# Optimization experiments

Measured on AMD Instinct MI355X. Metric: run time of the kernel, lower is better.

The kernel has to match this reference:

```python
import jax, jax.numpy as jnp
import numpy as np
from jax import lax

B, C_IN, H, W = 16, 2048, 16, 16
HIDDEN, N_ANC = 512, 9
N_POS, N_NEG = 2048, 2048
TOT = B * N_ANC * H * W  # 36864 = flat conf logits; also rows of reg.view(-1,4)


def _xyxy_to_cxcywh(b):
    x1, y1, x2, y2 = b[..., 0], b[..., 1], b[..., 2], b[..., 3]
    return jnp.stack([(x1 + x2) * 0.5, (y1 + y2) * 0.5, x2 - x1, y2 - y1], axis=-1)


def _cxcywh_to_xyxy(b):
    cx, cy, w, h = b[..., 0], b[..., 1], b[..., 2], b[..., 3]
    return jnp.stack([cx - w * 0.5, cy - h * 0.5, cx + w * 0.5, cy + h * 0.5], axis=-1)


def _rand_boxes(key, n):
    # valid xyxy boxes on the 16x16 feature-map coordinate grid, w,h in [1,4]
    k1, k2 = jax.random.split(key)
    xy = jax.random.uniform(k1, (n, 2), jnp.float32) * 12.0
    wh = 1.0 + jax.random.uniform(k2, (n, 2), jnp.float32) * 3.0
    return jnp.concatenate([xy, xy + wh], axis=-1)


def setup_inputs() -> dict:
    key = jax.random.key(0)
    ks = jax.random.split(key, 10)
    feature_map = jax.random.normal(ks[0], (B, C_IN, H, W), jnp.float32)
    pos_anc_ind = jax.random.randint(ks[1], (N_POS,), 0, TOT)
    neg_anc_ind = jax.random.randint(ks[2], (N_NEG,), 0, TOT)
    pos_anc_coords = _rand_boxes(ks[3], N_POS)
    gt_bboxes_pos = _rand_boxes(ks[4], N_POS)
    s1 = 1.0 / np.sqrt(C_IN * 9)
    W1 = jax.random.uniform(ks[5], (HIDDEN, C_IN, 3, 3), jnp.float32, -s1, s1)
    b1 = jnp.zeros((HIDDEN,), jnp.float32)
    s2 = 1.0 / np.sqrt(HIDDEN)
    Wc = jax.random.uniform(ks[6], (N_ANC, HIDDEN), jnp.float32, -s2, s2)
    bc = jnp.zeros((N_ANC,), jnp.float32)
    Wr = jax.random.uniform(ks[7], (N_ANC * 4, HIDDEN), jnp.float32, -s2, s2)
    br = jnp.zeros((N_ANC * 4,), jnp.float32)
    return {"feature_map": feature_map, "pos_anc_coords": pos_anc_coords,
            "gt_bboxes_pos": gt_bboxes_pos, "W1": W1, "b1": b1, "Wc": Wc,
            "bc": bc, "Wr": Wr, "br": br,
            "pos_anc_ind": pos_anc_ind, "neg_anc_ind": neg_anc_ind}


def generate_proposals(anchors, offsets):
    a = _xyxy_to_cxcywh(anchors)
    p = jnp.stack([a[:, 0] + offsets[:, 0] * a[:, 2],
                   a[:, 1] + offsets[:, 1] * a[:, 3],
                   a[:, 2] * jnp.exp(offsets[:, 2]),
                   a[:, 3] * jnp.exp(offsets[:, 3])], axis=-1)
    return _cxcywh_to_xyxy(p)


def calc_gt_offsets(anc, gt):
    a = _xyxy_to_cxcywh(anc)
    g = _xyxy_to_cxcywh(gt)
    tx = (g[:, 0] - a[:, 0]) / a[:, 2]
    ty = (g[:, 1] - a[:, 1]) / a[:, 3]
    tw = jnp.log(g[:, 2] / a[:, 2])
    th = jnp.log(g[:, 3] / a[:, 3])
    return jnp.stack([tx, ty, tw, th], axis=-1)


def reference(feature_map, pos_anc_coords, gt_bboxes_pos, W1, b1, Wc, bc, Wr, br,
              pos_anc_ind, neg_anc_ind):
    # ProposalModule: conv3x3 -> (dropout=identity in eval) -> relu -> 1x1 heads
    out = lax.conv_general_dilated(feature_map, W1, (1, 1), 'SAME',
                                   dimension_numbers=('NCHW', 'OIHW', 'NCHW'))
    out = jax.nn.relu(out + b1[None, :, None, None])
    conf = jnp.einsum('bchw,oc->bohw', out, Wc) + bc[None, :, None, None]   # [B,9,H,W]
    reg = jnp.einsum('bchw,oc->bohw', out, Wr) + br[None, :, None, None]    # [B,36,H,W]
    # irregular flat gathers, exactly mirroring torch .flatten()/.view(-1,4)
    conf_pos = conf.reshape(-1)[pos_anc_ind]
    conf_neg = conf.reshape(-1)[neg_anc_ind]
    offsets_pos = reg.reshape(-1, 4)[pos_anc_ind]
    proposals = generate_proposals(pos_anc_coords, offsets_pos)
    gt_offsets = calc_gt_offsets(pos_anc_coords, gt_bboxes_pos)
    # BCE-with-logits, targets 1 for pos / 0 for neg, reduction='sum' / B
    cls_loss = (jnp.sum(jax.nn.softplus(-conf_pos)) + jnp.sum(jax.nn.softplus(conf_neg))) / B
    # smooth L1 (beta=1), reduction='sum' / B
    d = offsets_pos - gt_offsets
    ad = jnp.abs(d)
    reg_loss = jnp.sum(jnp.where(ad < 1.0, 0.5 * d * d, ad - 0.5)) / B
    total_rpn_loss = 1.0 * cls_loss + 5.0 * reg_loss  # w_conf=1, w_reg=5
    return total_rpn_loss, proposals
```

## Files before the change

kernel.cpp:

```cpp
#include <hip/hip_runtime.h>
#include <hip/hip_bf16.h>
#include <stdint.h>

#define CIN 2048
#define HID 512
#define NPOS 2048
#define NNEG 2048

#define BM 256
#define BN 256
#define BK 32
#define NS 8
#define A_ELEMS (BM * BK)
#define B_ELEMS (BN * BK)

typedef __attribute__((ext_vector_type(8))) short s16x8;
typedef __attribute__((ext_vector_type(4))) short s16x4;
typedef __attribute__((ext_vector_type(4))) float f32x4;
typedef unsigned short ushort_t;

static __device__ __forceinline__ float bf2f(unsigned short u) {
    union { float f; unsigned int i; } v; v.i = ((unsigned int)u) << 16; return v.f;
}
static __device__ __forceinline__ unsigned short f2bf(float f) {
    union { float f; unsigned int i; } v; v.f = f;
    unsigned int r = v.i + 0x7FFF + ((v.i >> 16) & 1);
    return (unsigned short)(r >> 16);
}

typedef __attribute__((address_space(1))) const void gvoid_t;
typedef __attribute__((address_space(3))) void lvoid_t;
static __device__ __forceinline__ void gload16(const void* g, void* l) {
    __builtin_amdgcn_global_load_lds((gvoid_t*)g, (lvoid_t*)l, 16, 0, 0);
}

__global__ __launch_bounds__(256) void k_prep(const float* __restrict__ F,
                                              const float* __restrict__ W1,
                                              ushort_t* __restrict__ Fp,
                                              ushort_t* __restrict__ Wt2) {
    __shared__ float tile[64][17];
    __shared__ float buf[512 * 9];
    int bid = blockIdx.x;
    int t = threadIdx.x;
    if (bid < 256) {
        int b = bid >> 4, y = bid & 15;
        for (int ic0 = 0; ic0 < CIN; ic0 += 64) {
            {
                int ci = t >> 2, xg = t & 3;
                const float4 v = *(const float4*)&F[((size_t)(b * CIN + ic0 + ci) * 16 + y) * 16 + xg * 4];
                tile[ci][xg * 4 + 0] = v.x;
                tile[ci][xg * 4 + 1] = v.y;
                tile[ci][xg * 4 + 2] = v.z;
                tile[ci][xg * 4 + 3] = v.w;
            }
            __syncthreads();
            {
                int x = t >> 4, cig = t & 15;
                s16x4 o;
#pragma unroll
                for (int j = 0; j < 4; ++j) o[j] = (short)f2bf(tile[cig * 4 + j][x]);
                *(s16x4*)&Fp[((size_t)(b * 18 + y + 1) * 18 + (x + 1)) * CIN + ic0 + cig * 4] = o;
            }
            __syncthreads();
        }
    } else if (bid < 768) {
        int oc = bid - 256;
        for (int ic0 = 0; ic0 < CIN; ic0 += 512) {
            const float* src = W1 + ((size_t)oc * CIN + ic0) * 9;
            for (int i = t; i < 512 * 9; i += 256) buf[i] = src[i];
            __syncthreads();
            for (int s = t; s < 9 * 64; s += 256) {
                int k = s >> 6, g = s & 63;
                s16x8 v;
#pragma unroll
                for (int j = 0; j < 8; ++j) v[j] = (short)f2bf(buf[(g * 8 + j) * 9 + k]);
                *(s16x8*)&Wt2[((size_t)(k * HID + oc)) * CIN + ic0 + g * 8] = v;
            }
            __syncthreads();
        }
    } else {
        const s16x8 z = {0, 0, 0, 0, 0, 0, 0, 0};
        for (int idx = (bid - 768) * 256 + t; idx < 16 * 68 * 256; idx += 64 * 256) {
            int seg = idx & 255;
            int cell = (idx >> 8) % 68;
            int b = idx / (68 * 256);
            int Y, X;
            if (cell < 18)      { Y = 0;         X = cell; }
            else if (cell < 36) { Y = 17;        X = cell - 18; }
            else if (cell < 52) { Y = cell - 35; X = 0; }
            else                { Y = cell - 51; X = 17; }
            *(s16x8*)&Fp[((size_t)(b * 18 + Y) * 18 + X) * CIN + seg * 8] = z;
        }
    }
}

__global__ __launch_bounds__(512, 2) void k_gemm(const ushort_t* __restrict__ Fp,
                                                 const ushort_t* __restrict__ Wt2,
                                                 ushort_t* __restrict__ Part,
                                                 int icLen, int nPairs) {
    extern __shared__ ushort_t ldsbuf[];
    ushort_t* As = ldsbuf;
    ushort_t* Bs = ldsbuf + 4 * A_ELEMS;

    int bid = blockIdx.x;
    int rb = bid / nPairs;
    int pair = bid - rb * nPairs;
    int split = pair >> 1, cb = pair & 1;
    int icBase = split * icLen;
    int m0 = rb * BM, oc0 = cb * BN;
    int t = threadIdx.x;
    int wid = t >> 6, lane = t & 63;
    int wr = wid >> 2, wn = wid & 3;
    int hi = lane >> 4, lo = lane & 15;

    f32x4 acc[8][4];
#pragma unroll
    for (int a = 0; a < 8; ++a)
#pragma unroll
        for (int b = 0; b < 4; ++b) acc[a][b] = (f32x4){0.f, 0.f, 0.f, 0.f};

    int Abase[2], Bbase[2];
#pragma unroll
    for (int j = 0; j < 2; ++j) {
        int li = j * 512 + t;
        int row = li >> 2;
        int sg = (li & 3) ^ ((row >> 1) & 3);
        int m = m0 + row;
        int b = m >> 8, y = (m >> 4) & 15, x = m & 15;
        Abase[j] = ((b * 18 + y) * 18 + x) * CIN + sg * 8;
        Bbase[j] = (oc0 + row) * CIN + sg * 8;
    }
    int aidx[8], bidx[4];
#pragma unroll
    for (int fm = 0; fm < 8; ++fm) {
        int r = wr * 128 + fm * 16 + lo;
        aidx[fm] = r * BK + ((hi ^ ((r >> 1) & 3)) << 3);
    }
#pragma unroll
    for (int fn = 0; fn < 4; ++fn) {
        int rB = wn * 64 + fn * 16 + lo;
        bidx[fn] = rB * BK + ((hi ^ ((rB >> 1) & 3)) << 3);
    }

    const int nsteps = (icLen / BK) * 9;

#define STAGE(BUF, S)                                                                \
    do {                                                                             \
        int kidx_ = (S) % 9, icc_ = (S) / 9;                                         \
        int ak_ = ((kidx_ / 3) * 18 + (kidx_ - 3 * (kidx_ / 3))) * CIN + icBase + icc_ * BK; \
        int bk_ = kidx_ * HID * CIN + icBase + icc_ * BK;                            \
        ushort_t* dA_ = As + (BUF) * A_ELEMS;                                        \
        ushort_t* dB_ = Bs + (BUF) * B_ELEMS;                                        \
        _Pragma("unroll") for (int j_ = 0; j_ < 2; ++j_) {                           \
            gload16(Fp + Abase[j_] + ak_, dA_ + (size_t)(j_ * 512 + t) * 8);         \
            gload16(Wt2 + Bbase[j_] + bk_, dB_ + (size_t)(j_ * 512 + t) * 8);        \
        }                                                                            \
    } while (0)

    STAGE(0, 0); STAGE(1, 1); STAGE(2, 2);
    asm volatile("s_waitcnt vmcnt(8)" ::: "memory");
    __builtin_amdgcn_s_barrier();
    __builtin_amdgcn_sched_barrier(0);

#pragma unroll 1
    for (int step = 0; step < nsteps; ++step) {
        const ushort_t* cA = As + (step & 3) * A_ELEMS;
        const ushort_t* cB = Bs + (step & 3) * B_ELEMS;
        if (step + 3 < nsteps) STAGE((step + 3) & 3, step + 3);
        s16x8 af[8], bf[4];
#pragma unroll
        for (int fm = 0; fm < 8; ++fm) af[fm] = *(const s16x8*)&cA[aidx[fm]];
#pragma unroll
        for (int fn = 0; fn < 4; ++fn) bf[fn] = *(const s16x8*)&cB[bidx[fn]];
        __builtin_amdgcn_s_setprio(1);
#pragma unroll
        for (int fm = 0; fm < 8; ++fm)
#pragma unroll
            for (int fn = 0; fn < 4; ++fn)
                acc[fm][fn] = __builtin_amdgcn_mfma_f32_16x16x32_bf16(
                    af[fm], bf[fn], acc[fm][fn], 0, 0, 0);
        __builtin_amdgcn_s_setprio(0);
        if (step + 3 < nsteps) {
            asm volatile("s_waitcnt vmcnt(8)" ::: "memory");
            __builtin_amdgcn_s_barrier();
            __builtin_amdgcn_sched_barrier(0);
        } else if (step + 1 < nsteps) {
            asm volatile("s_waitcnt vmcnt(0)" ::: "memory");
            __builtin_amdgcn_s_barrier();
            __builtin_amdgcn_sched_barrier(0);
        }
    }
#undef STAGE

#pragma unroll
    for (int fm = 0; fm < 8; ++fm)
#pragma unroll
        for (int fn = 0; fn < 4; ++fn)
#pragma unroll
            for (int r = 0; r < 4; ++r) {
                int gm = m0 + wr * 128 + fm * 16 + hi * 4 + r;
                int gn = oc0 + wn * 64 + fn * 16 + lo;
                Part[((size_t)split * 4096 + gm) * HID + gn] = f2bf(acc[fm][fn][r]);
            }
}

__global__ __launch_bounds__(256) void k_heads(const ushort_t* __restrict__ Part, int ns,
                                               const float* __restrict__ b1,
                                               const float* __restrict__ Wc,
                                               const float* __restrict__ bc,
                                               const float* __restrict__ Wr,
                                               const float* __restrict__ br,
                                               float* __restrict__ conf,
                                               float* __restrict__ reg) {
    extern __shared__ ushort_t hsm[];
    ushort_t* Ah = hsm;
    ushort_t* Wh = hsm + 16 * HID;
    int t = threadIdx.x;
    int wid = t >> 6, lane = t & 63;
    int hi = lane >> 4, lo = lane & 15;
    int row0 = blockIdx.x * 16;

#pragma unroll
    for (int i = 0; i < 4; ++i) {
        int pos = i * 256 + t;
        int r = pos >> 6, sg = pos & 63;
        float s[8];
#pragma unroll
        for (int j = 0; j < 8; ++j) s[j] = 0.f;
        for (int sp = 0; sp < ns; ++sp) {
            s16x8 v = *(const s16x8*)&Part[((size_t)sp * 4096 + row0 + r) * HID + sg * 8];
#pragma unroll
            for (int j = 0; j < 8; ++j) s[j] += bf2f((unsigned short)v[j]);
        }
        s16x8 o;
#pragma unroll
        for (int j = 0; j < 8; ++j) o[j] = (short)f2bf(fmaxf(s[j] + b1[sg * 8 + j], 0.f));
        *(s16x8*)&Ah[r * HID + ((sg ^ (r & 7)) << 3)] = o;
    }
#pragma unroll
    for (int i = 0; i < 12; ++i) {
        int sid = i * 256 + t;
        int o = sid >> 6, sg = sid & 63;
        s16x8 v;
#pragma unroll
        for (int j = 0; j < 8; ++j) {
            float w = 0.f;
            if (o < 9) w = Wc[o * HID + sg * 8 + j];
            else if (o < 45) w = Wr[(size_t)(o - 9) * HID + sg * 8 + j];
            v[j] = (short)f2bf(w);
        }
        *(s16x8*)&Wh[o * HID + ((sg ^ (o & 7)) << 3)] = v;
    }
    __syncthreads();
    if (wid != 0) return;

    f32x4 acc[3];
#pragma unroll
    for (int fn = 0; fn < 3; ++fn) acc[fn] = (f32x4){0.f, 0.f, 0.f, 0.f};
#pragma unroll 1
    for (int kf = 0; kf < 16; ++kf) {
        int rA = lo;
        s16x8 a_ = *(const s16x8*)&Ah[rA * HID + ((kf * 32 + hi * 8) ^ ((rA & 7) << 3))];
#pragma unroll
        for (int fn = 0; fn < 3; ++fn) {
            int rB = fn * 16 + lo;
            s16x8 b_ = *(const s16x8*)&Wh[rB * HID + ((kf * 32 + hi * 8) ^ ((rB & 7) << 3))];
            acc[fn] = __builtin_amdgcn_mfma_f32_16x16x32_bf16(a_, b_, acc[fn], 0, 0, 0);
        }
    }
#pragma unroll
    for (int fn = 0; fn < 3; ++fn)
#pragma unroll
        for (int r = 0; r < 4; ++r) {
            int gm = row0 + hi * 4 + r;
            int o = fn * 16 + lo;
            float v = acc[fn][r];
            if (o < 9) conf[gm * 9 + o] = v + bc[o];
            else if (o < 45) reg[gm * 36 + (o - 9)] = v + br[o - 9];
        }
}

static __device__ __forceinline__ float softplus(float x) {
    return log1pf(expf(-fabsf(x))) + fmaxf(x, 0.f);
}

__global__ __launch_bounds__(1024) void k_loss(const float* __restrict__ conf,
                                               const float* __restrict__ reg,
                                               const int* __restrict__ pos_ind,
                                               const int* __restrict__ neg_ind,
                                               const float* __restrict__ anc,
                                               const float* __restrict__ gt,
                                               float* __restrict__ out) {
    int t = threadIdx.x;
    float cls = 0.f, rloss = 0.f;
    for (int p = t; p < NPOS; p += 1024) {
        int ind = pos_ind[p];
        {
            int b = ind / 2304, r = ind % 2304;
            int c = r >> 8, r2 = r & 255;
            float cv = conf[(b * 256 + r2) * 9 + c];
            cls += softplus(-cv);
        }
        float off[4];
#pragma unroll
        for (int j = 0; j < 4; ++j) {
            int e = 4 * ind + j;
            int b = e / 9216, r = e % 9216;
            int c = r >> 8, r2 = r & 255;
            off[j] = reg[(b * 256 + r2) * 36 + c];
        }
        float ax1 = anc[4 * p], ay1 = anc[4 * p + 1], ax2 = anc[4 * p + 2], ay2 = anc[4 * p + 3];
        float acx = (ax1 + ax2) * 0.5f, acy = (ay1 + ay2) * 0.5f;
        float aw = ax2 - ax1, ah = ay2 - ay1;
        float pcx = acx + off[0] * aw, pcy = acy + off[1] * ah;
        float pw = aw * expf(off[2]), ph = ah * expf(off[3]);
        out[1 + 4 * p + 0] = pcx - pw * 0.5f;
        out[1 + 4 * p + 1] = pcy - ph * 0.5f;
        out[1 + 4 * p + 2] = pcx + pw * 0.5f;
        out[1 + 4 * p + 3] = pcy + ph * 0.5f;
        float gx1 = gt[4 * p], gy1 = gt[4 * p + 1], gx2 = gt[4 * p + 2], gy2 = gt[4 * p + 3];
        float gcx = (gx1 + gx2) * 0.5f, gcy = (gy1 + gy2) * 0.5f;
        float gw = gx2 - gx1, gh = gy2 - gy1;
        float tv[4];
        tv[0] = (gcx - acx) / aw;
        tv[1] = (gcy - acy) / ah;
        tv[2] = logf(gw / aw);
        tv[3] = logf(gh / ah);
#pragma unroll
        for (int j = 0; j < 4; ++j) {
            float d = off[j] - tv[j];
            float ad = fabsf(d);
            rloss += (ad < 1.f) ? 0.5f * d * d : ad - 0.5f;
        }
    }
    for (int q = t; q < NNEG; q += 1024) {
        int ind = neg_ind[q];
        int b = ind / 2304, r = ind % 2304;
        int c = r >> 8, r2 = r & 255;
        float cv = conf[(b * 256 + r2) * 9 + c];
        cls += softplus(cv);
    }
    __shared__ float s1[1024], s2[1024];
    s1[t] = cls;
    s2[t] = rloss;
    __syncthreads();
    for (int s = 512; s > 0; s >>= 1) {
        if (t < s) {
            s1[t] += s1[t + s];
            s2[t] += s2[t + s];
        }
        __syncthreads();
    }
    if (t == 0) out[0] = (s1[0] + 5.f * s2[0]) / 16.f;
}

extern "C" void kernel_launch(void* const* d_in, const int* in_sizes, int n_in,
                              void* d_out, int out_size, void* d_ws, size_t ws_size,
                              hipStream_t stream) {
    const float* F   = (const float*)d_in[0];
    const float* anc = (const float*)d_in[1];
    const float* gt  = (const float*)d_in[2];
    const float* W1  = (const float*)d_in[3];
    const float* b1  = (const float*)d_in[4];
    const float* Wc  = (const float*)d_in[5];
    const float* bc  = (const float*)d_in[6];
    const float* Wr  = (const float*)d_in[7];
    const float* br  = (const float*)d_in[8];
    const int* pos_ind = (const int*)d_in[9];
    const int* neg_ind = (const int*)d_in[10];
    float* out = (float*)d_out;

    char* ws = (char*)d_ws;
    const size_t FP_BYTES   = (size_t)16 * 18 * 18 * CIN * 2;
    const size_t WT_BYTES   = (size_t)9 * HID * CIN * 2;
    const size_t PART_ONE   = (size_t)4096 * HID * 2;
    const size_t CONF_BYTES = (size_t)4096 * 9 * 4;

    int icLen = CIN / NS;

    ushort_t* Fp   = (ushort_t*)ws;
    ushort_t* Wt2  = (ushort_t*)(ws + FP_BYTES);
    ushort_t* Part = (ushort_t*)(ws + FP_BYTES + WT_BYTES);
    float* conf    = (float*)(ws + FP_BYTES + WT_BYTES + (size_t)NS * PART_ONE);
    float* reg     = (float*)(ws + FP_BYTES + WT_BYTES + (size_t)NS * PART_ONE + CONF_BYTES);

    const int GEMM_LDS = 4 * (A_ELEMS + B_ELEMS) * 2;
    hipFuncSetAttribute((const void*)k_gemm, hipFuncAttributeMaxDynamicSharedMemorySize, GEMM_LDS);
    const int HEADS_LDS = (16 + 48) * HID * 2;
    hipFuncSetAttribute((const void*)k_heads, hipFuncAttributeMaxDynamicSharedMemorySize, HEADS_LDS);

    k_prep<<<832, 256, 0, stream>>>(F, W1, Fp, Wt2);
    k_gemm<<<(4096 / BM) * (HID / BN) * NS, 512, GEMM_LDS, stream>>>(Fp, Wt2, Part, icLen, 2 * NS);
    k_heads<<<256, 256, HEADS_LDS, stream>>>(Part, NS, b1, Wc, bc, Wr, br, conf, reg);
    k_loss<<<1, 1024, 0, stream>>>(conf, reg, pos_ind, neg_ind, anc, gt, out);
}
```

Measured before the change: 134.5 us.

## Restructure conv GEMM main loop: BK=64 double buffer with interleaved quarter-stage loads

Doubles the K tile to 64 and drops from a 4-deep to a 2-deep LDS ring, keeping the same LDS footprint. Each step is split into four MFMA phases, and each phase is fenced by barriers and paired with one quarter of the next tile's global-to-LDS loads. The LDS swizzle changes to an 8-way XOR pattern to suit the wider rows. The weight-prep copy is also vectorised to float4. The aim is fewer loop iterations and barriers per unit of K, with loads spread across the compute. The cost is extra barriers inside each step and a shallower prefetch depth, which may expose memory latency.

```diff
diff --git a/kernel.cpp b/kernel.cpp
--- a/kernel.cpp
+++ b/kernel.cpp
@@ -9,7 +9,7 @@
 
 #define BM 256
 #define BN 256
-#define BK 32
+#define BK 64
 #define NS 8
 #define A_ELEMS (BM * BK)
 #define B_ELEMS (BN * BK)
@@ -67,7 +67,11 @@
         int oc = bid - 256;
         for (int ic0 = 0; ic0 < CIN; ic0 += 512) {
             const float* src = W1 + ((size_t)oc * CIN + ic0) * 9;
-            for (int i = t; i < 512 * 9; i += 256) buf[i] = src[i];
+            {
+                const float4* s4 = (const float4*)src;
+                float4* b4 = (float4*)buf;
+                for (int i = t; i < 1152; i += 256) b4[i] = s4[i];
+            }
             __syncthreads();
             for (int s = t; s < 9 * 64; s += 256) {
                 int k = s >> 6, g = s & 63;
@@ -100,7 +104,7 @@
                                                  int icLen, int nPairs) {
     extern __shared__ ushort_t ldsbuf[];
     ushort_t* As = ldsbuf;
-    ushort_t* Bs = ldsbuf + 4 * A_ELEMS;
+    ushort_t* Bs = ldsbuf + 2 * A_ELEMS;
 
     int bid = blockIdx.x;
     int rb = bid / nPairs;
@@ -119,78 +123,132 @@
 #pragma unroll
         for (int b = 0; b < 4; ++b) acc[a][b] = (f32x4){0.f, 0.f, 0.f, 0.f};
 
-    int Abase[2], Bbase[2];
-#pragma unroll
-    for (int j = 0; j < 2; ++j) {
+    int Abase[4], Bbase[4];
+#pragma unroll
+    for (int j = 0; j < 4; ++j) {
         int li = j * 512 + t;
-        int row = li >> 2;
-        int sg = (li & 3) ^ ((row >> 1) & 3);
+        int row = li >> 3;
+        int sg = (li & 7) ^ (row & 7);
         int m = m0 + row;
         int b = m >> 8, y = (m >> 4) & 15, x = m & 15;
         Abase[j] = ((b * 18 + y) * 18 + x) * CIN + sg * 8;
         Bbase[j] = (oc0 + row) * CIN + sg * 8;
     }
-    int aidx[8], bidx[4];
-#pragma unroll
-    for (int fm = 0; fm < 8; ++fm) {
-        int r = wr * 128 + fm * 16 + lo;
-        aidx[fm] = r * BK + ((hi ^ ((r >> 1) & 3)) << 3);
-    }
-#pragma unroll
-    for (int fn = 0; fn < 4; ++fn) {
-        int rB = wn * 64 + fn * 16 + lo;
-        bidx[fn] = rB * BK + ((hi ^ ((rB >> 1) & 3)) << 3);
-    }
+    int sw0 = (hi * 8) ^ ((lo & 7) << 3);
+    int sw1 = (32 + hi * 8) ^ ((lo & 7) << 3);
+    int arow = (wr * 128 + lo) * BK;
+    int brow = (wn * 64 + lo) * BK;
 
     const int nsteps = (icLen / BK) * 9;
 
-#define STAGE(BUF, S)                                                                \
+#define STAGE_PAIR(BUF, S, J)                                                        \
     do {                                                                             \
         int kidx_ = (S) % 9, icc_ = (S) / 9;                                         \
         int ak_ = ((kidx_ / 3) * 18 + (kidx_ - 3 * (kidx_ / 3))) * CIN + icBase + icc_ * BK; \
         int bk_ = kidx_ * HID * CIN + icBase + icc_ * BK;                            \
-        ushort_t* dA_ = As + (BUF) * A_ELEMS;                                        \
-        ushort_t* dB_ = Bs + (BUF) * B_ELEMS;                                        \
-        _Pragma("unroll") for (int j_ = 0; j_ < 2; ++j_) {                           \
-            gload16(Fp + Abase[j_] + ak_, dA_ + (size_t)(j_ * 512 + t) * 8);         \
-            gload16(Wt2 + Bbase[j_] + bk_, dB_ + (size_t)(j_ * 512 + t) * 8);        \
-        }                                                                            \
+        gload16(Fp + Abase[J] + ak_, As + (BUF) * A_ELEMS + (size_t)((J) * 512 + t) * 8); \
+        gload16(Wt2 + Bbase[J] + bk_, Bs + (BUF) * B_ELEMS + (size_t)((J) * 512 + t) * 8); \
     } while (0)
 
-    STAGE(0, 0); STAGE(1, 1); STAGE(2, 2);
-    asm volatile("s_waitcnt vmcnt(8)" ::: "memory");
+    STAGE_PAIR(0, 0, 0); STAGE_PAIR(0, 0, 1); STAGE_PAIR(0, 0, 2); STAGE_PAIR(0, 0, 3);
+    asm volatile("s_waitcnt vmcnt(0)" ::: "memory");
     __builtin_amdgcn_s_barrier();
     __builtin_amdgcn_sched_barrier(0);
 
 #pragma unroll 1
     for (int step = 0; step < nsteps; ++step) {
-        const ushort_t* cA = As + (step & 3) * A_ELEMS;
-        const ushort_t* cB = Bs + (step & 3) * B_ELEMS;
-        if (step + 3 < nsteps) STAGE((step + 3) & 3, step + 3);
-        s16x8 af[8], bf[4];
-#pragma unroll
-        for (int fm = 0; fm < 8; ++fm) af[fm] = *(const s16x8*)&cA[aidx[fm]];
-#pragma unroll
-        for (int fn = 0; fn < 4; ++fn) bf[fn] = *(const s16x8*)&cB[bidx[fn]];
+        int cur = step & 1;
+        const ushort_t* cA = As + cur * A_ELEMS;
+        const ushort_t* cB = Bs + cur * B_ELEMS;
+        bool st = (step + 1 < nsteps);
+        s16x8 af[4][2], bf[4][2];
+
+#pragma unroll
+        for (int fm = 0; fm < 4; ++fm) {
+            af[fm][0] = *(const s16x8*)&cA[arow + fm * 1024 + sw0];
+            af[fm][1] = *(const s16x8*)&cA[arow + fm * 1024 + sw1];
+        }
+#pragma unroll
+        for (int fn = 0; fn < 2; ++fn) {
+            bf[fn][0] = *(const s16x8*)&cB[brow + fn * 1024 + sw0];
+            bf[fn][1] = *(const s16x8*)&cB[brow + fn * 1024 + sw1];
+        }
+        if (st) STAGE_PAIR(cur ^ 1, step + 1, 0);
+        __builtin_amdgcn_s_barrier();
+        asm volatile("s_waitcnt lgkmcnt(0)" ::: "memory");
+        __builtin_amdgcn_sched_barrier(0);
         __builtin_amdgcn_s_setprio(1);
 #pragma unroll
-        for (int fm = 0; fm < 8; ++fm)
-#pragma unroll
-            for (int fn = 0; fn < 4; ++fn)
-                acc[fm][fn] = __builtin_amdgcn_mfma_f32_16x16x32_bf16(
-                    af[fm], bf[fn], acc[fm][fn], 0, 0, 0);
+        for (int fm = 0; fm < 4; ++fm)
+#pragma unroll
+            for (int fn = 0; fn < 2; ++fn)
+#pragma unroll
+                for (int ks = 0; ks < 2; ++ks)
+                    acc[fm][fn] = __builtin_amdgcn_mfma_f32_16x16x32_bf16(
+                        af[fm][ks], bf[fn][ks], acc[fm][fn], 0, 0, 0);
         __builtin_amdgcn_s_setprio(0);
-        if (step + 3 < nsteps) {
-            asm volatile("s_waitcnt vmcnt(8)" ::: "memory");
-            __builtin_amdgcn_s_barrier();
-            __builtin_amdgcn_sched_barrier(0);
-        } else if (step + 1 < nsteps) {
+        __builtin_amdgcn_s_barrier();
+
+#pragma unroll
+        for (int fn = 2; fn < 4; ++fn) {
+            bf[fn][0] = *(const s16x8*)&cB[brow + fn * 1024 + sw0];
+            bf[fn][1] = *(const s16x8*)&cB[brow + fn * 1024 + sw1];
+        }
+        if (st) STAGE_PAIR(cur ^ 1, step + 1, 1);
+        __builtin_amdgcn_s_barrier();
+        asm volatile("s_waitcnt lgkmcnt(0)" ::: "memory");
+        __builtin_amdgcn_sched_barrier(0);
+        __builtin_amdgcn_s_setprio(1);
+#pragma unroll
+        for (int fm = 0; fm < 4; ++fm)
+#pragma unroll
+            for (int fn = 2; fn < 4; ++fn)
+#pragma unroll
+                for (int ks = 0; ks < 2; ++ks)
+                    acc[fm][fn] = __builtin_amdgcn_mfma_f32_16x16x32_bf16(
+                        af[fm][ks], bf[fn][ks], acc[fm][fn], 0, 0, 0);
+        __builtin_amdgcn_s_setprio(0);
+        __builtin_amdgcn_s_barrier();
+
+#pragma unroll
+        for (int fm = 0; fm < 4; ++fm) {
+            af[fm][0] = *(const s16x8*)&cA[arow + (fm + 4) * 1024 + sw0];
+            af[fm][1] = *(const s16x8*)&cA[arow + (fm + 4) * 1024 + sw1];
+        }
+        if (st) STAGE_PAIR(cur ^ 1, step + 1, 2);
+        __builtin_amdgcn_s_barrier();
+        asm volatile("s_waitcnt lgkmcnt(0)" ::: "memory");
+        __builtin_amdgcn_sched_barrier(0);
+        __builtin_amdgcn_s_setprio(1);
+#pragma unroll
+        for (int fm = 0; fm < 4; ++fm)
+#pragma unroll
+            for (int fn = 0; fn < 2; ++fn)
+#pragma unroll
+                for (int ks = 0; ks < 2; ++ks)
+                    acc[4 + fm][fn] = __builtin_amdgcn_mfma_f32_16x16x32_bf16(
+                        af[fm][ks], bf[fn][ks], acc[4 + fm][fn], 0, 0, 0);
+        __builtin_amdgcn_s_setprio(0);
+        __builtin_amdgcn_s_barrier();
+
+        if (st) STAGE_PAIR(cur ^ 1, step + 1, 3);
+        __builtin_amdgcn_s_setprio(1);
+#pragma unroll
+        for (int fm = 0; fm < 4; ++fm)
+#pragma unroll
+            for (int fn = 2; fn < 4; ++fn)
+#pragma unroll
+                for (int ks = 0; ks < 2; ++ks)
+                    acc[4 + fm][fn] = __builtin_amdgcn_mfma_f32_16x16x32_bf16(
+                        af[fm][ks], bf[fn][ks], acc[4 + fm][fn], 0, 0, 0);
+        __builtin_amdgcn_s_setprio(0);
+        if (st) {
             asm volatile("s_waitcnt vmcnt(0)" ::: "memory");
             __builtin_amdgcn_s_barrier();
             __builtin_amdgcn_sched_barrier(0);
         }
     }
-#undef STAGE
+#undef STAGE_PAIR
 
 #pragma unroll
     for (int fm = 0; fm < 8; ++fm)
@@ -384,7 +442,7 @@
     float* conf    = (float*)(ws + FP_BYTES + WT_BYTES + (size_t)NS * PART_ONE);
     float* reg     = (float*)(ws + FP_BYTES + WT_BYTES + (size_t)NS * PART_ONE + CONF_BYTES);
 
-    const int GEMM_LDS = 4 * (A_ELEMS + B_ELEMS) * 2;
+    const int GEMM_LDS = 2 * (A_ELEMS + B_ELEMS) * 2;
     hipFuncSetAttribute((const void*)k_gemm, hipFuncAttributeMaxDynamicSharedMemorySize, GEMM_LDS);
     const int HEADS_LDS = (16 + 48) * HID * 2;
     hipFuncSetAttribute((const void*)k_heads, hipFuncAttributeMaxDynamicSharedMemorySize, HEADS_LDS);
```

Measured after the change: 135.1 us. No clear change (+0.4%).

## Load weight fragments directly from global, double BK, triple-buffer only activations in LDS

Applied to the files above, without the earlier changes.

The GEMM stops staging the weight (B) tile through LDS. Each wave now reads its B fragments straight from global memory into registers, while only the activation (A) tile goes through a 3-deep LDS ring with BK raised to 64 and a new XOR swizzle. This cuts LDS footprint and LDS traffic and halves the number of barrier steps, at the cost of uncoalesced-ish global B reads and more live registers. The prep kernel also vectorizes the W1 copy into LDS with float4 loads.

```diff
diff --git a/kernel.cpp b/kernel.cpp
--- a/kernel.cpp
+++ b/kernel.cpp
@@ -9,10 +9,9 @@
 
 #define BM 256
 #define BN 256
-#define BK 32
+#define BK 64
 #define NS 8
 #define A_ELEMS (BM * BK)
-#define B_ELEMS (BN * BK)
 
 typedef __attribute__((ext_vector_type(8))) short s16x8;
 typedef __attribute__((ext_vector_type(4))) short s16x4;
@@ -67,7 +66,11 @@
         int oc = bid - 256;
         for (int ic0 = 0; ic0 < CIN; ic0 += 512) {
             const float* src = W1 + ((size_t)oc * CIN + ic0) * 9;
-            for (int i = t; i < 512 * 9; i += 256) buf[i] = src[i];
+            {
+                const float4* s4 = (const float4*)src;
+                float4* b4 = (float4*)buf;
+                for (int i = t; i < 1152; i += 256) b4[i] = s4[i];
+            }
             __syncthreads();
             for (int s = t; s < 9 * 64; s += 256) {
                 int k = s >> 6, g = s & 63;
@@ -100,7 +103,6 @@
                                                  int icLen, int nPairs) {
     extern __shared__ ushort_t ldsbuf[];
     ushort_t* As = ldsbuf;
-    ushort_t* Bs = ldsbuf + 4 * A_ELEMS;
 
     int bid = blockIdx.x;
     int rb = bid / nPairs;
@@ -119,69 +121,74 @@
 #pragma unroll
         for (int b = 0; b < 4; ++b) acc[a][b] = (f32x4){0.f, 0.f, 0.f, 0.f};
 
-    int Abase[2], Bbase[2];
-#pragma unroll
-    for (int j = 0; j < 2; ++j) {
+    int Abase[4];
+#pragma unroll
+    for (int j = 0; j < 4; ++j) {
         int li = j * 512 + t;
-        int row = li >> 2;
-        int sg = (li & 3) ^ ((row >> 1) & 3);
+        int row = li >> 3;
+        int sg = (li & 7) ^ (row & 7);
         int m = m0 + row;
         int b = m >> 8, y = (m >> 4) & 15, x = m & 15;
         Abase[j] = ((b * 18 + y) * 18 + x) * CIN + sg * 8;
-        Bbase[j] = (oc0 + row) * CIN + sg * 8;
-    }
-    int aidx[8], bidx[4];
-#pragma unroll
-    for (int fm = 0; fm < 8; ++fm) {
-        int r = wr * 128 + fm * 16 + lo;
-        aidx[fm] = r * BK + ((hi ^ ((r >> 1) & 3)) << 3);
-    }
-#pragma unroll
-    for (int fn = 0; fn < 4; ++fn) {
-        int rB = wn * 64 + fn * 16 + lo;
-        bidx[fn] = rB * BK + ((hi ^ ((rB >> 1) & 3)) << 3);
-    }
+    }
+    int aidx[8][2];
+#pragma unroll
+    for (int fm = 0; fm < 8; ++fm)
+#pragma unroll
+        for (int ks = 0; ks < 2; ++ks) {
+            int r = wr * 128 + fm * 16 + lo;
+            aidx[fm][ks] = r * BK + ((ks * 32 + hi * 8) ^ ((r & 7) << 3));
+        }
+    int bRowBase = (oc0 + wn * 64 + lo) * CIN + hi * 8;
 
     const int nsteps = (icLen / BK) * 9;
 
-#define STAGE(BUF, S)                                                                \
+#define STAGE_A(BUF, S)                                                              \
     do {                                                                             \
         int kidx_ = (S) % 9, icc_ = (S) / 9;                                         \
         int ak_ = ((kidx_ / 3) * 18 + (kidx_ - 3 * (kidx_ / 3))) * CIN + icBase + icc_ * BK; \
-        int bk_ = kidx_ * HID * CIN + icBase + icc_ * BK;                            \
         ushort_t* dA_ = As + (BUF) * A_ELEMS;                                        \
-        ushort_t* dB_ = Bs + (BUF) * B_ELEMS;                                        \
-        _Pragma("unroll") for (int j_ = 0; j_ < 2; ++j_) {                           \
+        _Pragma("unroll") for (int j_ = 0; j_ < 4; ++j_)                             \
             gload16(Fp + Abase[j_] + ak_, dA_ + (size_t)(j_ * 512 + t) * 8);         \
-            gload16(Wt2 + Bbase[j_] + bk_, dB_ + (size_t)(j_ * 512 + t) * 8);        \
-        }                                                                            \
     } while (0)
 
-    STAGE(0, 0); STAGE(1, 1); STAGE(2, 2);
-    asm volatile("s_waitcnt vmcnt(8)" ::: "memory");
+    STAGE_A(0, 0); STAGE_A(1, 1);
+    asm volatile("s_waitcnt vmcnt(4)" ::: "memory");
     __builtin_amdgcn_s_barrier();
     __builtin_amdgcn_sched_barrier(0);
 
+    int bi = 0;
 #pragma unroll 1
     for (int step = 0; step < nsteps; ++step) {
-        const ushort_t* cA = As + (step & 3) * A_ELEMS;
-        const ushort_t* cB = Bs + (step & 3) * B_ELEMS;
-        if (step + 3 < nsteps) STAGE((step + 3) & 3, step + 3);
-        s16x8 af[8], bf[4];
-#pragma unroll
-        for (int fm = 0; fm < 8; ++fm) af[fm] = *(const s16x8*)&cA[aidx[fm]];
-#pragma unroll
-        for (int fn = 0; fn < 4; ++fn) bf[fn] = *(const s16x8*)&cB[bidx[fn]];
+        const ushort_t* cA = As + bi * A_ELEMS;
+        int b2 = (bi >= 1) ? bi - 1 : 2;
+        int kidx = step % 9, icc = step / 9;
+        int bpos = kidx * HID * CIN + icBase + icc * BK;
+
+        s16x8 bf[4][2];
+#pragma unroll
+        for (int fn = 0; fn < 4; ++fn)
+#pragma unroll
+            for (int ks = 0; ks < 2; ++ks)
+                bf[fn][ks] = *(const s16x8*)&Wt2[(size_t)bpos + bRowBase + fn * 16 * CIN + ks * 32];
+        if (step + 2 < nsteps) STAGE_A(b2, step + 2);
+        s16x8 af[8][2];
+#pragma unroll
+        for (int fm = 0; fm < 8; ++fm)
+#pragma unroll
+            for (int ks = 0; ks < 2; ++ks) af[fm][ks] = *(const s16x8*)&cA[aidx[fm][ks]];
         __builtin_amdgcn_s_setprio(1);
 #pragma unroll
         for (int fm = 0; fm < 8; ++fm)
 #pragma unroll
             for (int fn = 0; fn < 4; ++fn)
-                acc[fm][fn] = __builtin_amdgcn_mfma_f32_16x16x32_bf16(
-                    af[fm], bf[fn], acc[fm][fn], 0, 0, 0);
+#pragma unroll
+                for (int ks = 0; ks < 2; ++ks)
+                    acc[fm][fn] = __builtin_amdgcn_mfma_f32_16x16x32_bf16(
+                        af[fm][ks], bf[fn][ks], acc[fm][fn], 0, 0, 0);
         __builtin_amdgcn_s_setprio(0);
-        if (step + 3 < nsteps) {
-            asm volatile("s_waitcnt vmcnt(8)" ::: "memory");
+        if (step + 2 < nsteps) {
+            asm volatile("s_waitcnt vmcnt(4)" ::: "memory");
             __builtin_amdgcn_s_barrier();
             __builtin_amdgcn_sched_barrier(0);
         } else if (step + 1 < nsteps) {
@@ -189,8 +196,9 @@
             __builtin_amdgcn_s_barrier();
             __builtin_amdgcn_sched_barrier(0);
         }
-    }
-#undef STAGE
+        bi = (bi == 2) ? 0 : bi + 1;
+    }
+#undef STAGE_A
 
 #pragma unroll
     for (int fm = 0; fm < 8; ++fm)
@@ -384,7 +392,7 @@
     float* conf    = (float*)(ws + FP_BYTES + WT_BYTES + (size_t)NS * PART_ONE);
     float* reg     = (float*)(ws + FP_BYTES + WT_BYTES + (size_t)NS * PART_ONE + CONF_BYTES);
 
-    const int GEMM_LDS = 4 * (A_ELEMS + B_ELEMS) * 2;
+    const int GEMM_LDS = 3 * A_ELEMS * 2;
     hipFuncSetAttribute((const void*)k_gemm, hipFuncAttributeMaxDynamicSharedMemorySize, GEMM_LDS);
     const int HEADS_LDS = (16 + 48) * HID * 2;
     hipFuncSetAttribute((const void*)k_heads, hipFuncAttributeMaxDynamicSharedMemorySize, HEADS_LDS);
```

Result: slower. 173.7 us (+29.1%).
